# Kernel tuning notes

Hardware: AMD Instinct MI355X
Metric: run time of the kernel (lower is better)

## Reference

```python
import jax, jax.numpy as jnp
import numpy as np

N_NODES = 100000
N_EDGES = 1600000
D_FEAT = 128
HIDDEN = 128
OUT = 40


def setup_inputs() -> dict:
    key = jax.random.key(0)
    ks = jax.random.split(key, 8)
    x = jax.random.normal(ks[0], (N_NODES, D_FEAT), dtype=jnp.float32)
    edge_index = jax.random.randint(ks[1], (2, N_EDGES), 0, N_NODES, dtype=jnp.int64)
    s1 = 1.0 / np.sqrt(D_FEAT)
    s2 = 1.0 / np.sqrt(HIDDEN)
    Wl1 = jax.random.uniform(ks[2], (HIDDEN, D_FEAT), jnp.float32, -s1, s1)
    bl1 = jnp.zeros((HIDDEN,), jnp.float32)
    Wr1 = jax.random.uniform(ks[3], (HIDDEN, D_FEAT), jnp.float32, -s1, s1)
    Wl2 = jax.random.uniform(ks[4], (OUT, HIDDEN), jnp.float32, -s2, s2)
    bl2 = jnp.zeros((OUT,), jnp.float32)
    Wr2 = jax.random.uniform(ks[5], (OUT, HIDDEN), jnp.float32, -s2, s2)
    return {"x": x, "edge_index": edge_index, "Wl1": Wl1, "bl1": bl1,
            "Wr1": Wr1, "Wl2": Wl2, "bl2": bl2, "Wr2": Wr2}


def _sage_conv(x, src, dst, Wl, bl, Wr):
    # mean aggregation of source features into target nodes (PyG source_to_target)
    n = x.shape[0]
    agg = jax.ops.segment_sum(x[src], dst, num_segments=n)          # [N, d]
    cnt = jax.ops.segment_sum(jnp.ones((src.shape[0],), x.dtype), dst, num_segments=n)
    mean = agg / jnp.maximum(cnt, 1.0)[:, None]
    return mean @ Wl.T + bl + x @ Wr.T  # lin_l(agg) + lin_r(x)


def reference(x, edge_index, Wl1, bl1, Wr1, Wl2, bl2, Wr2):
    src, dst = edge_index[0], edge_index[1]
    h = _sage_conv(x, src, dst, Wl1, bl1, Wr1)
    h = jax.nn.relu(h)
    # dropout p=0.5 is identity in eval mode
    h = _sage_conv(h, src, dst, Wl2, bl2, Wr2)
    return h, jax.nn.log_softmax(h, axis=1)
```

## Files before the change

kernel.cpp:

```cpp
#include <hip/hip_runtime.h>
#include <hip/hip_bf16.h>
#include <hip/hip_fp8.h>
#include <math.h>
#include <stdint.h>

#define N_NODES 100000
#define N_EDGES 1600000
#define D 128
#define OUTC 40
#define M_PAD 100096
#define NSLICE 12500
#define SLOTS 64

#define FILL_BLOCKS 6256
#define CVT_X_BLOCKS 3128
#define MIX_BLOCKS 9384
#define CVT_W_BLOCKS 176

typedef __bf16 bf16;
typedef __bf16 bf16x2 __attribute__((ext_vector_type(2)));
typedef __bf16 bf16x4 __attribute__((ext_vector_type(4)));
typedef __bf16 bf16x8 __attribute__((ext_vector_type(8)));
typedef float f32x4 __attribute__((ext_vector_type(4)));
typedef uint32_t u32;
typedef uint8_t u8;

__device__ __forceinline__ void dec4(u32 w, float* o) {
    union { u32 u; __hip_fp8_e4m3 f[4]; } U; U.u = w;
    o[0] = (float)U.f[0]; o[1] = (float)U.f[1];
    o[2] = (float)U.f[2]; o[3] = (float)U.f[3];
}

__device__ __constant__ int LR24[24] = {0,0,-1, 0,0,-1, 0,0,-1, 1,0,-1,
                                        1,0,-1, 1,1,-1, 1,1,-1, 1,1,-1};

__global__ __launch_bounds__(256) void prep_fill(
    const float* __restrict__ x,
    const float* __restrict__ Wl1, const float* __restrict__ Wr1,
    const float* __restrict__ Wl2, const float* __restrict__ Wr2,
    const int* __restrict__ src, const int* __restrict__ dst,
    bf16* __restrict__ xb, u32* __restrict__ xq4,
    bf16* __restrict__ Wl1b, bf16* __restrict__ Wr1b,
    bf16* __restrict__ Wl2b, bf16* __restrict__ Wr2b,
    int* __restrict__ cur, int* __restrict__ eid) {
    int b = blockIdx.x;
    int t = threadIdx.x;
    if (b < MIX_BLOCKS) {
        int lr = LR24[b % 24];
        if (lr >= 0) {
            int part = b & 7;
            int chunk = (b / 24) * 2 + lr;
            int lo = part * NSLICE;
#pragma unroll
            for (int u = 0; u < 2; u++) {
                int e = chunk * 2048 + u * 1024 + t * 4;
                if (e + 4 <= N_EDGES) {
                    int4 d4 = *(const int4*)(dst + e);
                    int4 s4 = *(const int4*)(src + e);
                    if ((unsigned)(d4.x - lo) < (unsigned)NSLICE) {
                        int sl = atomicAdd(&cur[d4.x], 1);
                        if (sl < SLOTS) eid[(size_t)d4.x * SLOTS + sl] = s4.x;
                    }
                    if ((unsigned)(d4.y - lo) < (unsigned)NSLICE) {
                        int sl = atomicAdd(&cur[d4.y], 1);
                        if (sl < SLOTS) eid[(size_t)d4.y * SLOTS + sl] = s4.y;
                    }
                    if ((unsigned)(d4.z - lo) < (unsigned)NSLICE) {
                        int sl = atomicAdd(&cur[d4.z], 1);
                        if (sl < SLOTS) eid[(size_t)d4.z * SLOTS + sl] = s4.z;
                    }
                    if ((unsigned)(d4.w - lo) < (unsigned)NSLICE) {
                        int sl = atomicAdd(&cur[d4.w], 1);
                        if (sl < SLOTS) eid[(size_t)d4.w * SLOTS + sl] = s4.w;
                    }
                } else {
                    for (int k = e; k < N_EDGES && k < e + 4; k++) {
                        int d = dst[k];
                        if ((unsigned)(d - lo) < (unsigned)NSLICE) {
                            int sl = atomicAdd(&cur[d], 1);
                            if (sl < SLOTS) eid[(size_t)d * SLOTS + sl] = src[k];
                        }
                    }
                }
            }
        } else {
            int cb = b / 3;
#pragma unroll
            for (int k = 0; k < 4; k++) {
                size_t fidx = (size_t)cb * 1024 + k * 256 + t;
                size_t row = fidx >> 5;
                bf16x4 st;
                union { u32 u; __hip_fp8_e4m3 f[4]; } P;
                if (row < N_NODES) {
                    float4 v = *(const float4*)(x + fidx * 4);
                    st[0] = (bf16)v.x; st[1] = (bf16)v.y; st[2] = (bf16)v.z; st[3] = (bf16)v.w;
                    P.f[0] = __hip_fp8_e4m3(v.x); P.f[1] = __hip_fp8_e4m3(v.y);
                    P.f[2] = __hip_fp8_e4m3(v.z); P.f[3] = __hip_fp8_e4m3(v.w);
                } else {
                    st[0] = (bf16)0.f; st[1] = (bf16)0.f; st[2] = (bf16)0.f; st[3] = (bf16)0.f;
                    P.u = 0;
                }
                *(bf16x4*)(xb + fidx * 4) = st;
                xq4[fidx] = P.u;
            }
        }
    } else {
        int i = (b - MIX_BLOCKS) * 256 + t;
        if (i < 16384) {
            Wl1b[i] = (bf16)Wl1[i];
        } else if (i < 32768) {
            int j = i - 16384; Wr1b[j] = (bf16)Wr1[j];
        } else if (i < 38912) {
            int j = i - 32768; int r = j >> 7, k = j & 127;
            Wl2b[j] = (r < OUTC) ? (bf16)Wl2[r * D + k] : (bf16)0.f;
        } else {
            int j = i - 38912; int r = j >> 7, k = j & 127;
            Wr2b[j] = (r < OUTC) ? (bf16)Wr2[r * D + k] : (bf16)0.f;
        }
    }
}

__global__ __launch_bounds__(256) void gather_mean128(
    const u8* __restrict__ xq, const int* __restrict__ eid,
    const int* __restrict__ cur, bf16* __restrict__ meanb) {
    int node = blockIdx.x * 4 + (threadIdx.x >> 6);
    int lane = threadIdx.x & 63;
    int q = lane >> 4;
    int sl = lane & 15;
    if (node >= N_NODES) {
        if (q == 0) {
            bf16x8 zr;
#pragma unroll
            for (int j = 0; j < 8; j++) zr[j] = (bf16)0.f;
            *(bf16x8*)(meanb + (size_t)node * D + sl * 8) = zr;
        }
        return;
    }
    int cnt = cur[node];
    if (cnt > SLOTS) cnt = SLOTS;
    const int* ep = eid + (size_t)node * SLOTS;
    float inv = 1.f / fmaxf((float)cnt, 1.f);
    float acc[8];
#pragma unroll
    for (int j = 0; j < 8; j++) acc[j] = 0.f;
    const u8* base = xq + sl * 8;
    int e = 0;
    for (; e + 16 <= cnt; e += 16) {
        int s0 = ep[e + q], s1 = ep[e + 4 + q], s2 = ep[e + 8 + q], s3 = ep[e + 12 + q];
        uint2 w0 = *(const uint2*)(base + (size_t)s0 * D);
        uint2 w1 = *(const uint2*)(base + (size_t)s1 * D);
        uint2 w2 = *(const uint2*)(base + (size_t)s2 * D);
        uint2 w3 = *(const uint2*)(base + (size_t)s3 * D);
        float f0[8], f1[8], f2[8], f3[8];
        dec4(w0.x, f0); dec4(w0.y, f0 + 4);
        dec4(w1.x, f1); dec4(w1.y, f1 + 4);
        dec4(w2.x, f2); dec4(w2.y, f2 + 4);
        dec4(w3.x, f3); dec4(w3.y, f3 + 4);
#pragma unroll
        for (int j = 0; j < 8; j++) acc[j] += (f0[j] + f1[j]) + (f2[j] + f3[j]);
    }
    for (; e + 4 <= cnt; e += 4) {
        uint2 w = *(const uint2*)(base + (size_t)ep[e + q] * D);
        float f[8]; dec4(w.x, f); dec4(w.y, f + 4);
#pragma unroll
        for (int j = 0; j < 8; j++) acc[j] += f[j];
    }
    if (e + q < cnt) {
        uint2 w = *(const uint2*)(base + (size_t)ep[e + q] * D);
        float f[8]; dec4(w.x, f); dec4(w.y, f + 4);
#pragma unroll
        for (int j = 0; j < 8; j++) acc[j] += f[j];
    }
#pragma unroll
    for (int j = 0; j < 8; j++) {
        acc[j] += __shfl_xor(acc[j], 16);
        acc[j] += __shfl_xor(acc[j], 32);
    }
    if (q == 0) {
        bf16x8 st;
#pragma unroll
        for (int j = 0; j < 8; j++) st[j] = (bf16)(acc[j] * inv);
        *(bf16x8*)(meanb + (size_t)node * D + sl * 8) = st;
    }
}

#define SH_STRIDE 136
__global__ __launch_bounds__(256) void l12_mfma(
    const bf16* __restrict__ meanb, const bf16* __restrict__ xb,
    const bf16* __restrict__ Wl1b, const bf16* __restrict__ Wr1b,
    const float* __restrict__ bl1,
    const bf16* __restrict__ Wl2b, const bf16* __restrict__ Wr2b,
    const float* __restrict__ bl2,
    __hip_fp8_e4m3* __restrict__ h1pq, bf16* __restrict__ zb) {
    __shared__ bf16 sh1[256][SH_STRIDE];
    int wave = threadIdx.x >> 6;
    int lane = threadIdx.x & 63;
    int rowBase = blockIdx.x * 256 + wave * 64;
    int rloc = wave * 64;
    int lr = lane & 15;
    int kg = lane >> 4;

    f32x4 acc[4][8];
#pragma unroll
    for (int r = 0; r < 4; r++)
#pragma unroll
        for (int jf = 0; jf < 8; jf++) acc[r][jf] = (f32x4){0.f, 0.f, 0.f, 0.f};

#define K_HALF(A, W)                                                                   \
    {                                                                                  \
        _Pragma("unroll") for (int ks = 0; ks < 4; ks++) {                             \
            int k0 = ks * 32 + kg * 8;                                                 \
            bf16x8 bfrag[8];                                                           \
            _Pragma("unroll") for (int jf = 0; jf < 8; jf++)                           \
                bfrag[jf] = *(const bf16x8*)((W) + (size_t)(jf * 16 + lr) * D + k0);   \
            _Pragma("unroll") for (int r = 0; r < 4; r++) {                            \
                bf16x8 afrag = *(const bf16x8*)((A) + (size_t)(rowBase + r * 16 + lr) * D + k0); \
                _Pragma("unroll") for (int jf = 0; jf < 8; jf++)                       \
                    acc[r][jf] = __builtin_amdgcn_mfma_f32_16x16x32_bf16(              \
                        afrag, bfrag[jf], acc[r][jf], 0, 0, 0);                        \
            }                                                                          \
        }                                                                              \
    }
    K_HALF(meanb, Wl1b)
    K_HALF(xb, Wr1b)
#undef K_HALF

#pragma unroll
    for (int jf = 0; jf < 8; jf++) {
        int col = jf * 16 + lr;
        float bb = bl1[col];
#pragma unroll
        for (int r = 0; r < 4; r++) {
#pragma unroll
            for (int q = 0; q < 4; q++) {
                sh1[rloc + r * 16 + kg * 4 + q][col] = (bf16)fmaxf(acc[r][jf][q] + bb, 0.f);
            }
        }
    }

    f32x4 accL[4][3], accR[4][3];
#pragma unroll
    for (int r = 0; r < 4; r++)
#pragma unroll
        for (int jf = 0; jf < 3; jf++) {
            accL[r][jf] = (f32x4){0.f, 0.f, 0.f, 0.f};
            accR[r][jf] = (f32x4){0.f, 0.f, 0.f, 0.f};
        }
#pragma unroll
    for (int ks = 0; ks < 4; ks++) {
        int k0 = ks * 32 + kg * 8;
        bf16x8 bfl[3], bfr[3];
#pragma unroll
        for (int jf = 0; jf < 3; jf++) {
            bfl[jf] = *(const bf16x8*)(Wl2b + (size_t)(jf * 16 + lr) * D + k0);
            bfr[jf] = *(const bf16x8*)(Wr2b + (size_t)(jf * 16 + lr) * D + k0);
        }
#pragma unroll
        for (int r = 0; r < 4; r++) {
            bf16x8 afrag = *(const bf16x8*)&sh1[rloc + r * 16 + lr][k0];
#pragma unroll
            for (int jf = 0; jf < 3; jf++) {
                accL[r][jf] = __builtin_amdgcn_mfma_f32_16x16x32_bf16(afrag, bfl[jf], accL[r][jf], 0, 0, 0);
                accR[r][jf] = __builtin_amdgcn_mfma_f32_16x16x32_bf16(afrag, bfr[jf], accR[r][jf], 0, 0, 0);
            }
        }
    }
#pragma unroll
    for (int jf = 0; jf < 3; jf++) {
        int col = jf * 16 + lr;
        bool cok = col < OUTC;
        float bias = cok ? bl2[col] : 0.f;
#pragma unroll
        for (int r = 0; r < 4; r++) {
#pragma unroll
            for (int q = 0; q < 4; q++) {
                int row = rowBase + r * 16 + kg * 4 + q;
                if (cok && row < N_NODES) {
                    h1pq[(size_t)row * OUTC + col] = __hip_fp8_e4m3(accL[r][jf][q]);
                    zb[(size_t)row * OUTC + col] = (bf16)(accR[r][jf][q] + bias);
                }
            }
        }
    }
}

__global__ __launch_bounds__(256) void gather40_final(
    const u8* __restrict__ h1pq, const int* __restrict__ eid,
    const int* __restrict__ cur, const bf16* __restrict__ zb,
    float* __restrict__ h2, float* __restrict__ lsm) {
    int node = blockIdx.x * 4 + (threadIdx.x >> 6);
    int lane = threadIdx.x & 63;
    int g = lane / 10;
    int f = lane - g * 10;
    int cnt = cur[node];
    if (cnt > SLOTS) cnt = SLOTS;
    const int* ep = eid + (size_t)node * SLOTS;
    float inv = 1.f / fmaxf((float)cnt, 1.f);
    float a[4] = {0.f, 0.f, 0.f, 0.f};
    if (g < 6) {
        const u8* base = h1pq + f * 4;
        int e = g;
        for (; e + 6 < cnt; e += 12) {
            u32 w0 = *(const u32*)(base + (size_t)ep[e] * OUTC);
            u32 w1 = *(const u32*)(base + (size_t)ep[e + 6] * OUTC);
            float t0[4], t1[4];
            dec4(w0, t0); dec4(w1, t1);
#pragma unroll
            for (int j = 0; j < 4; j++) a[j] += t0[j] + t1[j];
        }
        if (e < cnt) {
            u32 w = *(const u32*)(base + (size_t)ep[e] * OUTC);
            float t[4]; dec4(w, t);
#pragma unroll
            for (int j = 0; j < 4; j++) a[j] += t[j];
        }
    }
#pragma unroll
    for (int j = 0; j < 4; j++) {
        a[j] += __shfl(a[j], lane + 30);
        a[j] += __shfl(a[j], lane + 10) + __shfl(a[j], lane + 20);
    }
    bool act = lane < 10;
    float v[4];
    float m = -INFINITY;
    if (act) {
        size_t o = (size_t)node * OUTC + f * 4;
        bf16x4 zz = *(const bf16x4*)(zb + o);
#pragma unroll
        for (int j = 0; j < 4; j++) v[j] = a[j] * inv + (float)zz[j];
        m = fmaxf(fmaxf(v[0], v[1]), fmaxf(v[2], v[3]));
    }
#pragma unroll
    for (int s = 8; s >= 1; s >>= 1) m = fmaxf(m, __shfl_xor(m, s, 16));
    float ssum = 0.f;
    if (act) ssum = expf(v[0] - m) + expf(v[1] - m) + expf(v[2] - m) + expf(v[3] - m);
#pragma unroll
    for (int s = 8; s >= 1; s >>= 1) ssum += __shfl_xor(ssum, s, 16);
    if (act) {
        float ls = m + logf(ssum);
        size_t o = (size_t)node * OUTC + f * 4;
        *(float4*)(h2 + o) = make_float4(v[0], v[1], v[2], v[3]);
        *(float4*)(lsm + o) = make_float4(v[0] - ls, v[1] - ls, v[2] - ls, v[3] - ls);
    }
}

extern "C" void kernel_launch(void* const* d_in, const int* in_sizes, int n_in,
                              void* d_out, int out_size, void* d_ws, size_t ws_size,
                              hipStream_t stream) {
    const float* x   = (const float*)d_in[0];
    const int*   ei  = (const int*)d_in[1];
    const float* Wl1 = (const float*)d_in[2];
    const float* bl1 = (const float*)d_in[3];
    const float* Wr1 = (const float*)d_in[4];
    const float* Wl2 = (const float*)d_in[5];
    const float* bl2 = (const float*)d_in[6];
    const float* Wr2 = (const float*)d_in[7];

    const int* src = ei;
    const int* dst = ei + N_EDGES;

    char* W = (char*)d_ws;
    bf16* xb    = (bf16*)W;            W += (size_t)M_PAD * D * 2;
    bf16* meanb = (bf16*)W;            W += (size_t)M_PAD * D * 2;
    u8*   xq    = (u8*)W;              W += (size_t)M_PAD * D;
    u8*   h1pq  = (u8*)W;              W += (size_t)N_NODES * OUTC;
    bf16* zb    = (bf16*)W;            W += (size_t)N_NODES * OUTC * 2;
    bf16* Wl1b  = (bf16*)W;            W += 16384 * 2;
    bf16* Wr1b  = (bf16*)W;            W += 16384 * 2;
    bf16* Wl2b  = (bf16*)W;            W += 48 * D * 2;
    bf16* Wr2b  = (bf16*)W;            W += 48 * D * 2;
    int*  eid   = (int*)W;             W += (size_t)N_NODES * SLOTS * 4;
    int*  cur   = (int*)W;             W += (size_t)N_NODES * 4;

    float* h2  = (float*)d_out;
    float* lsm = h2 + (size_t)N_NODES * OUTC;

    hipMemsetAsync(cur, 0, N_NODES * sizeof(int), stream);

    prep_fill<<<MIX_BLOCKS + CVT_W_BLOCKS, 256, 0, stream>>>(
        x, Wl1, Wr1, Wl2, Wr2, src, dst,
        xb, (u32*)xq, Wl1b, Wr1b, Wl2b, Wr2b, cur, eid);

    gather_mean128<<<M_PAD / 4, 256, 0, stream>>>(xq, eid, cur, meanb);

    l12_mfma<<<M_PAD / 256, 256, 0, stream>>>(meanb, xb, Wl1b, Wr1b, bl1,
                                              Wl2b, Wr2b, bl2,
                                              (__hip_fp8_e4m3*)h1pq, zb);

    gather40_final<<<N_NODES / 4, 256, 0, stream>>>(h1pq, eid, cur, zb, h2, lsm);
}
```

Baseline: 232.5 us.

## Fuse layer-1 mean gather into MFMA kernel and use fp8 for root term

Merges the per-node mean aggregation kernel into the layer-1/layer-2 MFMA kernel: each block gathers 256 nodes' neighbor means into shared memory, then runs the GEMMs from there. This removes the meanb round trip through global memory. The bf16 copy of x is dropped and the x@Wr1 term now uses fp8 MFMA on the existing fp8 x and an fp8-quantized Wr1, which lowers precision. The risk is a much lower grid size: only about 391 blocks doing gather, with one thread walking a node's neighbor list serially, which may hurt latency hiding.

```diff
diff --git a/kernel.cpp b/kernel.cpp
--- a/kernel.cpp
+++ b/kernel.cpp
@@ -18,17 +18,20 @@
 #define CVT_W_BLOCKS 176
 
 typedef __bf16 bf16;
-typedef __bf16 bf16x2 __attribute__((ext_vector_type(2)));
 typedef __bf16 bf16x4 __attribute__((ext_vector_type(4)));
 typedef __bf16 bf16x8 __attribute__((ext_vector_type(8)));
 typedef float f32x4 __attribute__((ext_vector_type(4)));
 typedef uint32_t u32;
 typedef uint8_t u8;
+typedef long long i64;
 
 __device__ __forceinline__ void dec4(u32 w, float* o) {
     union { u32 u; __hip_fp8_e4m3 f[4]; } U; U.u = w;
     o[0] = (float)U.f[0]; o[1] = (float)U.f[1];
     o[2] = (float)U.f[2]; o[3] = (float)U.f[3];
+}
+__device__ __forceinline__ void dec16(uint4 w, float* o) {
+    dec4(w.x, o); dec4(w.y, o + 4); dec4(w.z, o + 8); dec4(w.w, o + 12);
 }
 
 __device__ __constant__ int LR24[24] = {0,0,-1, 0,0,-1, 0,0,-1, 1,0,-1,
@@ -39,8 +42,8 @@
     const float* __restrict__ Wl1, const float* __restrict__ Wr1,
     const float* __restrict__ Wl2, const float* __restrict__ Wr2,
     const int* __restrict__ src, const int* __restrict__ dst,
-    bf16* __restrict__ xb, u32* __restrict__ xq4,
-    bf16* __restrict__ Wl1b, bf16* __restrict__ Wr1b,
+    u32* __restrict__ xq4,
+    bf16* __restrict__ Wl1b, u8* __restrict__ Wr1q,
     bf16* __restrict__ Wl2b, bf16* __restrict__ Wr2b,
     int* __restrict__ cur, int* __restrict__ eid) {
     int b = blockIdx.x;
@@ -89,18 +92,14 @@
             for (int k = 0; k < 4; k++) {
                 size_t fidx = (size_t)cb * 1024 + k * 256 + t;
                 size_t row = fidx >> 5;
-                bf16x4 st;
                 union { u32 u; __hip_fp8_e4m3 f[4]; } P;
                 if (row < N_NODES) {
                     float4 v = *(const float4*)(x + fidx * 4);
-                    st[0] = (bf16)v.x; st[1] = (bf16)v.y; st[2] = (bf16)v.z; st[3] = (bf16)v.w;
                     P.f[0] = __hip_fp8_e4m3(v.x); P.f[1] = __hip_fp8_e4m3(v.y);
                     P.f[2] = __hip_fp8_e4m3(v.z); P.f[3] = __hip_fp8_e4m3(v.w);
                 } else {
-                    st[0] = (bf16)0.f; st[1] = (bf16)0.f; st[2] = (bf16)0.f; st[3] = (bf16)0.f;
                     P.u = 0;
                 }
-                *(bf16x4*)(xb + fidx * 4) = st;
                 xq4[fidx] = P.u;
             }
         }
@@ -109,7 +108,8 @@
         if (i < 16384) {
             Wl1b[i] = (bf16)Wl1[i];
         } else if (i < 32768) {
-            int j = i - 16384; Wr1b[j] = (bf16)Wr1[j];
+            int j = i - 16384;
+            Wr1q[j] = __hip_fp8_e4m3(Wr1[j]).__x;
         } else if (i < 38912) {
             int j = i - 32768; int r = j >> 7, k = j & 127;
             Wl2b[j] = (r < OUTC) ? (bf16)Wl2[r * D + k] : (bf16)0.f;
@@ -120,110 +120,103 @@
     }
 }
 
-__global__ __launch_bounds__(256) void gather_mean128(
+#define SH_STRIDE 136
+__global__ __launch_bounds__(256) void gather_l12(
     const u8* __restrict__ xq, const int* __restrict__ eid,
-    const int* __restrict__ cur, bf16* __restrict__ meanb) {
-    int node = blockIdx.x * 4 + (threadIdx.x >> 6);
-    int lane = threadIdx.x & 63;
-    int q = lane >> 4;
-    int sl = lane & 15;
-    if (node >= N_NODES) {
-        if (q == 0) {
-            bf16x8 zr;
-#pragma unroll
-            for (int j = 0; j < 8; j++) zr[j] = (bf16)0.f;
-            *(bf16x8*)(meanb + (size_t)node * D + sl * 8) = zr;
-        }
-        return;
-    }
-    int cnt = cur[node];
-    if (cnt > SLOTS) cnt = SLOTS;
-    const int* ep = eid + (size_t)node * SLOTS;
-    float inv = 1.f / fmaxf((float)cnt, 1.f);
-    float acc[8];
-#pragma unroll
-    for (int j = 0; j < 8; j++) acc[j] = 0.f;
-    const u8* base = xq + sl * 8;
-    int e = 0;
-    for (; e + 16 <= cnt; e += 16) {
-        int s0 = ep[e + q], s1 = ep[e + 4 + q], s2 = ep[e + 8 + q], s3 = ep[e + 12 + q];
-        uint2 w0 = *(const uint2*)(base + (size_t)s0 * D);
-        uint2 w1 = *(const uint2*)(base + (size_t)s1 * D);
-        uint2 w2 = *(const uint2*)(base + (size_t)s2 * D);
-        uint2 w3 = *(const uint2*)(base + (size_t)s3 * D);
-        float f0[8], f1[8], f2[8], f3[8];
-        dec4(w0.x, f0); dec4(w0.y, f0 + 4);
-        dec4(w1.x, f1); dec4(w1.y, f1 + 4);
-        dec4(w2.x, f2); dec4(w2.y, f2 + 4);
-        dec4(w3.x, f3); dec4(w3.y, f3 + 4);
-#pragma unroll
-        for (int j = 0; j < 8; j++) acc[j] += (f0[j] + f1[j]) + (f2[j] + f3[j]);
-    }
-    for (; e + 4 <= cnt; e += 4) {
-        uint2 w = *(const uint2*)(base + (size_t)ep[e + q] * D);
-        float f[8]; dec4(w.x, f); dec4(w.y, f + 4);
-#pragma unroll
-        for (int j = 0; j < 8; j++) acc[j] += f[j];
-    }
-    if (e + q < cnt) {
-        uint2 w = *(const uint2*)(base + (size_t)ep[e + q] * D);
-        float f[8]; dec4(w.x, f); dec4(w.y, f + 4);
-#pragma unroll
-        for (int j = 0; j < 8; j++) acc[j] += f[j];
-    }
-#pragma unroll
-    for (int j = 0; j < 8; j++) {
-        acc[j] += __shfl_xor(acc[j], 16);
-        acc[j] += __shfl_xor(acc[j], 32);
-    }
-    if (q == 0) {
-        bf16x8 st;
-#pragma unroll
-        for (int j = 0; j < 8; j++) st[j] = (bf16)(acc[j] * inv);
-        *(bf16x8*)(meanb + (size_t)node * D + sl * 8) = st;
-    }
-}
-
-#define SH_STRIDE 136
-__global__ __launch_bounds__(256) void l12_mfma(
-    const bf16* __restrict__ meanb, const bf16* __restrict__ xb,
-    const bf16* __restrict__ Wl1b, const bf16* __restrict__ Wr1b,
+    const int* __restrict__ cur,
+    const bf16* __restrict__ Wl1b, const u8* __restrict__ Wr1q,
     const float* __restrict__ bl1,
     const bf16* __restrict__ Wl2b, const bf16* __restrict__ Wr2b,
     const float* __restrict__ bl2,
     __hip_fp8_e4m3* __restrict__ h1pq, bf16* __restrict__ zb) {
-    __shared__ bf16 sh1[256][SH_STRIDE];
-    int wave = threadIdx.x >> 6;
-    int lane = threadIdx.x & 63;
-    int rowBase = blockIdx.x * 256 + wave * 64;
+    __shared__ bf16 sh[256][SH_STRIDE];
+    int t = threadIdx.x;
+    int rowBase = blockIdx.x * 256;
+
+    for (int ss = 0; ss < 8; ss++) {
+        int slot = ss * 256 + t;
+        int n = slot >> 3;
+        int sl = slot & 7;
+        int node = rowBase + n;
+        float acc[16];
+#pragma unroll
+        for (int j = 0; j < 16; j++) acc[j] = 0.f;
+        if (node < N_NODES) {
+            int cnt = cur[node];
+            if (cnt > SLOTS) cnt = SLOTS;
+            const int* ep = eid + (size_t)node * SLOTS;
+            const u8* base = xq + sl * 16;
+            int e = 0;
+            for (; e + 4 <= cnt; e += 4) {
+                int s0 = ep[e], s1 = ep[e + 1], s2 = ep[e + 2], s3 = ep[e + 3];
+                uint4 w0 = *(const uint4*)(base + (size_t)s0 * D);
+                uint4 w1 = *(const uint4*)(base + (size_t)s1 * D);
+                uint4 w2 = *(const uint4*)(base + (size_t)s2 * D);
+                uint4 w3 = *(const uint4*)(base + (size_t)s3 * D);
+                float f0[16], f1[16], f2[16], f3[16];
+                dec16(w0, f0); dec16(w1, f1); dec16(w2, f2); dec16(w3, f3);
+#pragma unroll
+                for (int j = 0; j < 16; j++) acc[j] += (f0[j] + f1[j]) + (f2[j] + f3[j]);
+            }
+            for (; e < cnt; e++) {
+                uint4 w = *(const uint4*)(base + (size_t)ep[e] * D);
+                float f[16]; dec16(w, f);
+#pragma unroll
+                for (int j = 0; j < 16; j++) acc[j] += f[j];
+            }
+            float inv = 1.f / fmaxf((float)cnt, 1.f);
+#pragma unroll
+            for (int j = 0; j < 16; j++) acc[j] *= inv;
+        }
+        bf16x8 st0, st1;
+#pragma unroll
+        for (int j = 0; j < 8; j++) { st0[j] = (bf16)acc[j]; st1[j] = (bf16)acc[8 + j]; }
+        *(bf16x8*)&sh[n][sl * 16] = st0;
+        *(bf16x8*)&sh[n][sl * 16 + 8] = st1;
+    }
+    __syncthreads();
+
+    int wave = t >> 6;
+    int lane = t & 63;
     int rloc = wave * 64;
     int lr = lane & 15;
     int kg = lane >> 4;
-
     f32x4 acc[4][8];
 #pragma unroll
     for (int r = 0; r < 4; r++)
 #pragma unroll
         for (int jf = 0; jf < 8; jf++) acc[r][jf] = (f32x4){0.f, 0.f, 0.f, 0.f};
 
-#define K_HALF(A, W)                                                                   \
-    {                                                                                  \
-        _Pragma("unroll") for (int ks = 0; ks < 4; ks++) {                             \
-            int k0 = ks * 32 + kg * 8;                                                 \
-            bf16x8 bfrag[8];                                                           \
-            _Pragma("unroll") for (int jf = 0; jf < 8; jf++)                           \
-                bfrag[jf] = *(const bf16x8*)((W) + (size_t)(jf * 16 + lr) * D + k0);   \
-            _Pragma("unroll") for (int r = 0; r < 4; r++) {                            \
-                bf16x8 afrag = *(const bf16x8*)((A) + (size_t)(rowBase + r * 16 + lr) * D + k0); \
-                _Pragma("unroll") for (int jf = 0; jf < 8; jf++)                       \
-                    acc[r][jf] = __builtin_amdgcn_mfma_f32_16x16x32_bf16(              \
-                        afrag, bfrag[jf], acc[r][jf], 0, 0, 0);                        \
-            }                                                                          \
-        }                                                                              \
-    }
-    K_HALF(meanb, Wl1b)
-    K_HALF(xb, Wr1b)
-#undef K_HALF
+#pragma unroll
+    for (int ks = 0; ks < 4; ks++) {
+        int k0 = ks * 32 + kg * 8;
+        bf16x8 bfrag[8];
+#pragma unroll
+        for (int jf = 0; jf < 8; jf++)
+            bfrag[jf] = *(const bf16x8*)(Wl1b + (size_t)(jf * 16 + lr) * D + k0);
+#pragma unroll
+        for (int r = 0; r < 4; r++) {
+            bf16x8 afrag = *(const bf16x8*)&sh[rloc + r * 16 + lr][k0];
+#pragma unroll
+            for (int jf = 0; jf < 8; jf++)
+                acc[r][jf] = __builtin_amdgcn_mfma_f32_16x16x32_bf16(afrag, bfrag[jf], acc[r][jf], 0, 0, 0);
+        }
+    }
+#pragma unroll
+    for (int ks = 0; ks < 4; ks++) {
+        int k0 = ks * 32 + kg * 8;
+        i64 bfr[8];
+#pragma unroll
+        for (int jf = 0; jf < 8; jf++)
+            bfr[jf] = *(const i64*)(Wr1q + (size_t)(jf * 16 + lr) * D + k0);
+#pragma unroll
+        for (int r = 0; r < 4; r++) {
+            i64 af = *(const i64*)(xq + (size_t)(rowBase + rloc + r * 16 + lr) * D + k0);
+#pragma unroll
+            for (int jf = 0; jf < 8; jf++)
+                acc[r][jf] = __builtin_amdgcn_mfma_f32_16x16x32_fp8_fp8(af, bfr[jf], acc[r][jf], 0, 0, 0);
+        }
+    }
 
 #pragma unroll
     for (int jf = 0; jf < 8; jf++) {
@@ -233,7 +226,7 @@
         for (int r = 0; r < 4; r++) {
 #pragma unroll
             for (int q = 0; q < 4; q++) {
-                sh1[rloc + r * 16 + kg * 4 + q][col] = (bf16)fmaxf(acc[r][jf][q] + bb, 0.f);
+                sh[rloc + r * 16 + kg * 4 + q][col] = (bf16)fmaxf(acc[r][jf][q] + bb, 0.f);
             }
         }
     }
@@ -249,19 +242,19 @@
 #pragma unroll
     for (int ks = 0; ks < 4; ks++) {
         int k0 = ks * 32 + kg * 8;
-        bf16x8 bfl[3], bfr[3];
+        bf16x8 bfl[3], bfr2[3];
 #pragma unroll
         for (int jf = 0; jf < 3; jf++) {
             bfl[jf] = *(const bf16x8*)(Wl2b + (size_t)(jf * 16 + lr) * D + k0);
-            bfr[jf] = *(const bf16x8*)(Wr2b + (size_t)(jf * 16 + lr) * D + k0);
-        }
-#pragma unroll
-        for (int r = 0; r < 4; r++) {
-            bf16x8 afrag = *(const bf16x8*)&sh1[rloc + r * 16 + lr][k0];
+            bfr2[jf] = *(const bf16x8*)(Wr2b + (size_t)(jf * 16 + lr) * D + k0);
+        }
+#pragma unroll
+        for (int r = 0; r < 4; r++) {
+            bf16x8 afrag = *(const bf16x8*)&sh[rloc + r * 16 + lr][k0];
 #pragma unroll
             for (int jf = 0; jf < 3; jf++) {
                 accL[r][jf] = __builtin_amdgcn_mfma_f32_16x16x32_bf16(afrag, bfl[jf], accL[r][jf], 0, 0, 0);
-                accR[r][jf] = __builtin_amdgcn_mfma_f32_16x16x32_bf16(afrag, bfr[jf], accR[r][jf], 0, 0, 0);
+                accR[r][jf] = __builtin_amdgcn_mfma_f32_16x16x32_bf16(afrag, bfr2[jf], accR[r][jf], 0, 0, 0);
             }
         }
     }
@@ -274,7 +267,7 @@
         for (int r = 0; r < 4; r++) {
 #pragma unroll
             for (int q = 0; q < 4; q++) {
-                int row = rowBase + r * 16 + kg * 4 + q;
+                int row = rowBase + rloc + r * 16 + kg * 4 + q;
                 if (cok && row < N_NODES) {
                     h1pq[(size_t)row * OUTC + col] = __hip_fp8_e4m3(accL[r][jf][q]);
                     zb[(size_t)row * OUTC + col] = (bf16)(accR[r][jf][q] + bias);
@@ -360,13 +353,11 @@
     const int* dst = ei + N_EDGES;
 
     char* W = (char*)d_ws;
-    bf16* xb    = (bf16*)W;            W += (size_t)M_PAD * D * 2;
-    bf16* meanb = (bf16*)W;            W += (size_t)M_PAD * D * 2;
     u8*   xq    = (u8*)W;              W += (size_t)M_PAD * D;
     u8*   h1pq  = (u8*)W;              W += (size_t)N_NODES * OUTC;
     bf16* zb    = (bf16*)W;            W += (size_t)N_NODES * OUTC * 2;
     bf16* Wl1b  = (bf16*)W;            W += 16384 * 2;
-    bf16* Wr1b  = (bf16*)W;            W += 16384 * 2;
+    u8*   Wr1q  = (u8*)W;              W += 16384;
     bf16* Wl2b  = (bf16*)W;            W += 48 * D * 2;
     bf16* Wr2b  = (bf16*)W;            W += 48 * D * 2;
     int*  eid   = (int*)W;             W += (size_t)N_NODES * SLOTS * 4;
@@ -379,13 +370,11 @@
 
     prep_fill<<<MIX_BLOCKS + CVT_W_BLOCKS, 256, 0, stream>>>(
         x, Wl1, Wr1, Wl2, Wr2, src, dst,
-        xb, (u32*)xq, Wl1b, Wr1b, Wl2b, Wr2b, cur, eid);
-
-    gather_mean128<<<M_PAD / 4, 256, 0, stream>>>(xq, eid, cur, meanb);
-
-    l12_mfma<<<M_PAD / 256, 256, 0, stream>>>(meanb, xb, Wl1b, Wr1b, bl1,
-                                              Wl2b, Wr2b, bl2,
-                                              (__hip_fp8_e4m3*)h1pq, zb);
+        (u32*)xq, Wl1b, Wr1q, Wl2b, Wr2b, cur, eid);
+
+    gather_l12<<<M_PAD / 256, 256, 0, stream>>>(
+        xq, eid, cur, Wl1b, Wr1q, bl1, Wl2b, Wr2b, bl2,
+        (__hip_fp8_e4m3*)h1pq, zb);
 
     gather40_final<<<N_NODES / 4, 256, 0, stream>>>(h1pq, eid, cur, zb, h2, lsm);
 }
```

Result: slower. 276.6 us (+19.0%).
